# Optimization experiments

Measured on AMD Instinct MI355X. Metric: run time of the kernel, lower is better.

Reference implementation:

```python
import jax, jax.numpy as jnp
import numpy as np

C, INTER, RED4 = 256, 128, 64  # in_channels, inter_ch=max(C//2,32), C//4

def setup_inputs() -> dict:
    key = jax.random.key(0)
    ks = jax.random.split(key, 12)
    B, H, W = 8, 64, 64
    s = 0.02
    return {
        "x": jax.random.normal(ks[0], (B, C, H, W), dtype=jnp.float32),
        "theta_w": jax.random.normal(ks[1], (INTER, C), dtype=jnp.float32) * s,
        "phi_w": jax.random.normal(ks[2], (INTER, C), dtype=jnp.float32) * s,
        "g_w": jax.random.normal(ks[3], (INTER, C), dtype=jnp.float32) * s,
        "out_w": jax.random.normal(ks[4], (C, INTER), dtype=jnp.float32) * s,
        "bn_gamma": jnp.ones((C,), dtype=jnp.float32),
        "bn_beta": jnp.zeros((C,), dtype=jnp.float32),
        "fc1_w": jax.random.normal(ks[5], (RED4, C), dtype=jnp.float32) * s,
        "fc1_b": jnp.zeros((RED4,), dtype=jnp.float32),
        "fc2_w": jax.random.normal(ks[6], (C, RED4), dtype=jnp.float32) * s,
        "fc2_b": jnp.zeros((C,), dtype=jnp.float32),
    }

def reference(x, theta_w, phi_w, g_w, out_w, bn_gamma, bn_beta, fc1_w, fc1_b, fc2_w, fc2_b):
    B, Cc, H, W = x.shape
    N = H * W
    xf = x.reshape(B, Cc, N)                              # [B,C,N]
    # 1x1 convs == per-pixel matmuls
    theta = jnp.einsum('ic,bcn->bni', theta_w, xf)        # [B,N,I]
    phi = jnp.einsum('ic,bcn->bin', phi_w, xf)            # [B,I,N]
    g = jnp.einsum('ic,bcn->bni', g_w, xf)                # [B,N,I]
    scale = 1.0 / jnp.sqrt(jnp.asarray(theta.shape[-1], theta.dtype))
    attn = jax.nn.softmax(jnp.einsum('bni,bim->bnm', theta, phi) * scale, axis=-1)  # [B,N,N]
    out = jnp.einsum('bnm,bmi->bni', attn, g)             # [B,N,I]
    out = jnp.einsum('ci,bni->bcn', out_w, out).reshape(B, Cc, H, W)
    # BatchNorm2d (training mode: batch stats, biased variance, eps=1e-5)
    mean = out.mean(axis=(0, 2, 3))
    var = out.var(axis=(0, 2, 3))
    out = (out - mean[:, None, None]) * jax.lax.rsqrt(var[:, None, None] + 1e-5)
    out = out * bn_gamma[:, None, None] + bn_beta[:, None, None]
    # SE channel attention on the input x
    pooled = x.mean(axis=(2, 3))                          # [B,C]
    h = jax.nn.relu(pooled @ fc1_w.T + fc1_b)
    ch_w = jax.nn.sigmoid(h @ fc2_w.T + fc2_b)[:, :, None, None]
    return x + out * ch_w
```

## Files before the change

### kernel.cpp

```cpp
#include <hip/hip_runtime.h>

#define B_DIM 8
#define C_DIM 256
#define I_DIM 128
#define N_DIM 4096
#define R_DIM 64

typedef unsigned short u16;
typedef unsigned int u32;
typedef __attribute__((ext_vector_type(8))) __bf16 bf16x8;
typedef __attribute__((ext_vector_type(4))) float f32x4;
typedef __attribute__((ext_vector_type(16))) float f32x16;

union BF8 { u32 u[4]; bf16x8 v; };

__device__ __forceinline__ u16 f2bf(float f) {
    union { float f; u32 u; } v; v.f = f;
    u32 r = v.u + 0x7FFFu + ((v.u >> 16) & 1u);
    return (u16)(r >> 16);
}
__device__ __forceinline__ float bf2f(u16 h) {
    union { u32 u; float f; } v; v.u = (u32)h << 16; return v.f;
}
__device__ __forceinline__ u32 pk2(float a, float b) {
    return (u32)f2bf(a) | ((u32)f2bf(b) << 16);
}
__device__ __forceinline__ u32 pk2t(float a, float b) {
    union { float f; u32 u; } ua, ub; ua.f = a; ub.f = b;
    return __builtin_amdgcn_perm(ub.u, ua.u, 0x07060302u);
}
__device__ __forceinline__ void async16(const u16* g, u16* l) {
    __builtin_amdgcn_global_load_lds((const __attribute__((address_space(1))) void*)g,
                                     (__attribute__((address_space(3))) void*)l, 16, 0, 0);
}

#define TH_SCALE 0.1275204890136f

static constexpr size_t OFF_BNSUM = 0;
static constexpr size_t OFF_BNSQ  = 1024;
static constexpr size_t OFF_POOL  = 2048;
static constexpr size_t OFF_CHW   = 10240;
static constexpr size_t OFF_W3    = 18432;
static constexpr size_t OFF_OWB   = 215040;
static constexpr size_t OFF_AO0   = 280576;
static constexpr size_t OFF_AO1   = OFF_AO0 + 8388608;
static constexpr size_t OFF_THETA = OFF_AO1 + 8388608;
static constexpr size_t OFF_PHIT  = OFF_THETA + 8388608;
static constexpr size_t OFF_GT    = OFF_PHIT + 8388608;
static constexpr size_t OFF_L0    = OFF_GT + 8388608;
static constexpr size_t OFF_L1    = OFF_L0 + 131072;
static constexpr size_t OFF_OUT2  = OFF_L1 + 131072;

__global__ void prep_kernel(const float* __restrict__ tw, const float* __restrict__ pw,
                            const float* __restrict__ gw, const float* __restrict__ ow,
                            u16* __restrict__ w3, u16* __restrict__ owb,
                            float* __restrict__ bnzero, float* __restrict__ pooled) {
    int idx = blockIdx.x * 256 + threadIdx.x;
    if (idx < 512) bnzero[idx] = 0.f;
    if (idx < 2048) pooled[idx] = 0.f;
    if (idx < 3 * 32768) {
        const float* src = idx < 32768 ? tw : (idx < 65536 ? pw : gw);
        w3[idx] = f2bf(src[idx & 32767]);
    }
    if (idx < 32768) owb[idx] = f2bf(ow[idx]);
}

__global__ void se_kernel(const float* __restrict__ pooled,
                          const float* __restrict__ fc1w, const float* __restrict__ fc1b,
                          const float* __restrict__ fc2w, const float* __restrict__ fc2b,
                          float* __restrict__ chw) {
    int b = blockIdx.x, t = threadIdx.x;
    __shared__ float sp[C_DIM], sh[R_DIM];
    sp[t] = pooled[b * C_DIM + t] * (1.f / N_DIM);
    __syncthreads();
    if (t < R_DIM) {
        float a = fc1b[t];
        for (int c = 0; c < C_DIM; ++c) a += sp[c] * fc1w[t * C_DIM + c];
        sh[t] = a > 0.f ? a : 0.f;
    }
    __syncthreads();
    float a = fc2b[t];
    for (int j = 0; j < R_DIM; ++j) a += sh[j] * fc2w[t * R_DIM + j];
    chw[b * C_DIM + t] = 1.f / (1.f + __builtin_amdgcn_exp2f(-a * 1.44269504089f));
}

__global__ __launch_bounds__(256) void qkv_kernel(const float* __restrict__ x,
                                                  const u16* __restrict__ w3,
                                                  u16* __restrict__ theta,
                                                  u16* __restrict__ phiT,
                                                  u16* __restrict__ gT,
                                                  float* __restrict__ pooled) {
    const int bid = blockIdx.x;
    const int b = bid & 7, nt = bid >> 3;
    const int n0 = nt * 64;
    const int t = threadIdx.x, lane = t & 63, w = t >> 6;
    const int cl = lane & 31, h = lane >> 5;

    __shared__ u16 As[64 * 256];
    __shared__ u16 Ep[128 * 72];

    {
        const float* xb = x + ((size_t)b * C_DIM) * N_DIM + n0;
        for (int it = 0; it < 16; ++it) {
            int id = it * 256 + t;
            int c = id >> 4, l16 = id & 15;
            float4 v = *(const float4*)(xb + (size_t)c * N_DIM + l16 * 4);
            int g = c >> 3, co = c & 7;
            float vv[4] = {v.x, v.y, v.z, v.w};
            #pragma unroll
            for (int k = 0; k < 4; ++k) {
                int n = l16 * 4 + k;
                As[n * 256 + ((g ^ (n & 7)) << 3) + co] = f2bf(vv[k]);
            }
            float s = (v.x + v.y) + (v.z + v.w);
            s += __shfl_xor(s, 1); s += __shfl_xor(s, 2);
            s += __shfl_xor(s, 4); s += __shfl_xor(s, 8);
            if ((t & 15) == 0) atomicAdd(&pooled[b * C_DIM + c], s);
        }
    }
    __syncthreads();

    const int mt = w & 1;
    const int ip = w >> 1;
    bf16x8 afr[16];
    #pragma unroll
    for (int ks = 0; ks < 16; ++ks) {
        int r = mt * 32 + cl;
        int g = 2 * ks + h;
        afr[ks] = *(const bf16x8*)&As[r * 256 + ((g ^ (r & 7)) << 3)];
    }

    for (int z = 0; z < 3; ++z) {
        const u16* wz = w3 + z * (I_DIM * C_DIM);
        f32x16 acc[2] = {};
        #pragma unroll
        for (int ks = 0; ks < 16; ++ks) {
            #pragma unroll
            for (int f = 0; f < 2; ++f) {
                int irow = (2 * ip + f) * 32 + cl;
                bf16x8 bfr = *(const bf16x8*)(wz + (size_t)irow * C_DIM + ks * 16 + h * 8);
                acc[f] = __builtin_amdgcn_mfma_f32_32x32x16_bf16(afr[ks], bfr, acc[f], 0, 0, 0);
            }
        }
        if (z < 2) {
            float sc = (z == 0) ? TH_SCALE : 1.0f;
            #pragma unroll
            for (int f = 0; f < 2; ++f) {
                int i = (2 * ip + f) * 32 + cl;
                #pragma unroll
                for (int r2 = 0; r2 < 4; ++r2)
                    #pragma unroll
                    for (int e = 0; e < 4; ++e) {
                        int n = mt * 32 + 8 * r2 + 4 * h + e;
                        Ep[n * 136 + i] = f2bf(acc[f][4 * r2 + e] * sc);
                    }
            }
            __syncthreads();
            u16* dst = (z == 0) ? theta : phiT;
            #pragma unroll
            for (int it = 0; it < 4; ++it) {
                int id = it * 256 + t;
                int n = id >> 4, l16 = id & 15;
                f32x4 vv = *(const f32x4*)&Ep[n * 136 + l16 * 8];
                *(f32x4*)(dst + ((size_t)(b * N_DIM) + n0 + n) * I_DIM + l16 * 8) = vv;
            }
            __syncthreads();
        } else {
            #pragma unroll
            for (int f = 0; f < 2; ++f) {
                int i = (2 * ip + f) * 32 + cl;
                #pragma unroll
                for (int r2 = 0; r2 < 4; ++r2) {
                    u32 lo = pk2(acc[f][4 * r2 + 0], acc[f][4 * r2 + 1]);
                    u32 hi = pk2(acc[f][4 * r2 + 2], acc[f][4 * r2 + 3]);
                    int nb = mt * 32 + 8 * r2 + 4 * h;
                    *(u32*)&Ep[i * 72 + nb] = lo;
                    *(u32*)&Ep[i * 72 + nb + 2] = hi;
                }
            }
            __syncthreads();
            #pragma unroll
            for (int it = 0; it < 4; ++it) {
                int id = it * 256 + t;
                int i = id >> 3, l8 = id & 7;
                f32x4 vv = *(const f32x4*)&Ep[i * 72 + l8 * 8];
                *(f32x4*)(gT + ((size_t)(b * I_DIM) + i) * N_DIM + n0 + l8 * 8) = vv;
            }
        }
    }
}

__global__ __launch_bounds__(256) void attn_kernel(const u16* __restrict__ theta,
                                                   const u16* __restrict__ phiT,
                                                   const u16* __restrict__ gT,
                                                   u16* __restrict__ ao0, u16* __restrict__ ao1,
                                                   float* __restrict__ l0, float* __restrict__ l1) {
    const int bid = blockIdx.x;
    const int b = bid & 7, mh = (bid >> 3) & 1, qt = bid >> 4;
    const int t = threadIdx.x, lane = t & 63, w = t >> 6;
    const int cl = lane & 31, h = lane >> 5;
    const int qw = qt * 128 + w * 32;

    __shared__ u16 SM[32768];
    __shared__ float lex[4][32];

    bf16x8 qf[8];
    {
        const u16* qp = theta + ((size_t)(b * N_DIM) + qw + cl) * I_DIM + h * 8;
        #pragma unroll
        for (int ks = 0; ks < 8; ++ks) qf[ks] = *(const bf16x8*)(qp + ks * 16);
    }

    const u16* kbase = phiT + (size_t)b * N_DIM * I_DIM + (size_t)(mh * 2048) * I_DIM;
    const u16* vbase = gT + (size_t)b * I_DIM * N_DIM + mh * 2048;
    const u16* kptr[4]; const u16* vptr[4];
    #pragma unroll
    for (int it = 0; it < 4; ++it) {
        int gi = (w * 4 + it) * 64 + lane;
        int kr = gi >> 4, kg = gi & 15;
        kptr[it] = kbase + (size_t)kr * I_DIM + ((kg ^ (kr & 7)) << 3);
        int vr = gi >> 3, vg = gi & 7;
        vptr[it] = vbase + (size_t)vr * N_DIM + ((vg ^ (vr & 7)) << 3);
    }

    auto issue = [&](int p) {
        u16* Kd = SM + p * 16384;
        u16* Vd = SM + p * 16384 + 8192;
        #pragma unroll
        for (int it = 0; it < 4; ++it) { async16(kptr[it], Kd + (w * 4 + it) * 512); kptr[it] += 64 * I_DIM; }
        #pragma unroll
        for (int it = 0; it < 4; ++it) { async16(vptr[it], Vd + (w * 4 + it) * 512); vptr[it] += 64; }
    };

    float lsum = 0.f;
    f32x16 O[4] = {};

    issue(0);

    for (int mc = 0; mc < 32; ++mc) {
        const int p = mc & 1;
        __asm__ volatile("s_barrier" ::: "memory");
        if (mc < 31) {
            issue(1 - p);
            __asm__ volatile("s_waitcnt vmcnt(8)" ::: "memory");
        } else {
            __asm__ volatile("s_waitcnt vmcnt(0)" ::: "memory");
        }
        __asm__ volatile("s_barrier" ::: "memory");

        const u16* Ks = SM + p * 16384;
        const u16* Vs = SM + p * 16384 + 8192;

        u32 pk[8][2];
        #pragma unroll
        for (int mt2 = 0; mt2 < 2; ++mt2) {
            f32x16 S = {};
            #pragma unroll
            for (int ks = 0; ks < 8; ++ks) {
                int r = mt2 * 32 + cl;
                bf16x8 kf = *(const bf16x8*)&Ks[r * 128 + (((2 * ks + h) ^ (r & 7)) << 3)];
                S = __builtin_amdgcn_mfma_f32_32x32x16_bf16(kf, qf[ks], S, 0, 0, 0);
            }
            #pragma unroll
            for (int r2 = 0; r2 < 4; ++r2) {
                float p0 = __builtin_amdgcn_exp2f(S[4 * r2 + 0]);
                float p1 = __builtin_amdgcn_exp2f(S[4 * r2 + 1]);
                float p2 = __builtin_amdgcn_exp2f(S[4 * r2 + 2]);
                float p3 = __builtin_amdgcn_exp2f(S[4 * r2 + 3]);
                lsum += (p0 + p1) + (p2 + p3);
                pk[mt2 * 4 + r2][0] = pk2t(p0, p1);
                pk[mt2 * 4 + r2][1] = pk2t(p2, p3);
            }
        }

        #pragma unroll
        for (int ks = 0; ks < 4; ++ks) {
            u32 a0 = pk[2 * ks][0], a1 = pk[2 * ks][1];
            u32 b0 = pk[2 * ks + 1][0], b1 = pk[2 * ks + 1][1];
            bool hb = (h != 0);
            u32 own0 = hb ? b0 : a0, own1 = hb ? b1 : a1;
            u32 xf0 = hb ? a0 : b0, xf1 = hb ? a1 : b1;
            u32 rc0 = (u32)__shfl_xor((int)xf0, 32);
            u32 rc1 = (u32)__shfl_xor((int)xf1, 32);
            BF8 A;
            A.u[0] = hb ? rc0 : own0;
            A.u[1] = hb ? rc1 : own1;
            A.u[2] = hb ? own0 : rc0;
            A.u[3] = hb ? own1 : rc1;
            #pragma unroll
            for (int f = 0; f < 4; ++f) {
                int ir = f * 32 + cl;
                bf16x8 vf = *(const bf16x8*)&Vs[ir * 64 + (((2 * ks + h) ^ (ir & 7)) << 3)];
                O[f] = __builtin_amdgcn_mfma_f32_32x32x16_bf16(A.v, vf, O[f], 0, 0, 0);
            }
        }
    }

    lsum += __shfl_xor(lsum, 32);
    if (h == 0) lex[w][cl] = lsum;
    __asm__ volatile("s_waitcnt lgkmcnt(0)" ::: "memory");

    float linv[16];
    {
        float* lw = lex[w];
        #pragma unroll
        for (int r2 = 0; r2 < 4; ++r2) {
            f32x4 lv = *(const f32x4*)&lw[8 * r2 + 4 * h];
            #pragma unroll
            for (int e = 0; e < 4; ++e) linv[4 * r2 + e] = 1.f / lv[e];
        }
    }

    u16* aop = (mh == 0) ? ao0 : ao1;
    float* lp = (mh == 0) ? l0 : l1;
    if (h == 0) lp[(size_t)b * N_DIM + qw + cl] = lsum;

    u16* ep = SM + w * 4096;
    #pragma unroll
    for (int f = 0; f < 4; ++f)
        #pragma unroll
        for (int r2 = 0; r2 < 4; ++r2)
            #pragma unroll
            for (int e = 0; e < 4; ++e) {
                int q = 8 * r2 + 4 * h + e;
                ep[q * 128 + f * 32 + cl] = f2bf(O[f][4 * r2 + e] * linv[4 * r2 + e]);
            }
    __asm__ volatile("s_waitcnt lgkmcnt(0)" ::: "memory");
    #pragma unroll
    for (int it = 0; it < 8; ++it) {
        int id = it * 64 + lane;
        int q = id >> 4, l16 = id & 15;
        f32x4 vv = *(const f32x4*)&ep[q * 128 + l16 * 8];
        *(f32x4*)(aop + ((size_t)(b * N_DIM) + qw + q) * I_DIM + l16 * 8) = vv;
    }
}

__global__ __launch_bounds__(256) void oproj_kernel(const u16* __restrict__ ao0,
                                                    const u16* __restrict__ ao1,
                                                    const float* __restrict__ l0,
                                                    const float* __restrict__ l1,
                                                    const u16* __restrict__ owb,
                                                    u16* __restrict__ out2,
                                                    float* __restrict__ bnsum,
                                                    float* __restrict__ bnsumsq) {
    const int bid = blockIdx.x;
    const int b = bid & 7, nt = bid >> 3;
    const int n0 = nt * 64;
    const int t = threadIdx.x, lane = t & 63, w = t >> 6;
    const int cl = lane & 31, h = lane >> 5;

    __shared__ u16 Ep[256 * 72];
    __shared__ float lsum[C_DIM], lsq[C_DIM];
    lsum[t] = 0.f; lsq[t] = 0.f;
    __syncthreads();

    const int mt = w & 1;
    const int nn = n0 + mt * 32 + cl;
    float w0, w1;
    {
        float la = l0[(size_t)b * N_DIM + nn], lb = l1[(size_t)b * N_DIM + nn];
        float inv = 1.f / (la + lb);
        w0 = la * inv; w1 = lb * inv;
    }
    bf16x8 afr[8];
    {
        const u16* p0 = ao0 + ((size_t)(b * N_DIM) + nn) * I_DIM + h * 8;
        const u16* p1 = ao1 + ((size_t)(b * N_DIM) + nn) * I_DIM + h * 8;
        #pragma unroll
        for (int ks = 0; ks < 8; ++ks) {
            bf16x8 x0 = *(const bf16x8*)(p0 + ks * 16);
            bf16x8 x1 = *(const bf16x8*)(p1 + ks * 16);
            const u16* u0 = (const u16*)&x0;
            const u16* u1 = (const u16*)&x1;
            float c0 = w0 * bf2f(u0[0]) + w1 * bf2f(u1[0]);
            float c1 = w0 * bf2f(u0[1]) + w1 * bf2f(u1[1]);
            float c2 = w0 * bf2f(u0[2]) + w1 * bf2f(u1[2]);
            float c3 = w0 * bf2f(u0[3]) + w1 * bf2f(u1[3]);
            float c4 = w0 * bf2f(u0[4]) + w1 * bf2f(u1[4]);
            float c5 = w0 * bf2f(u0[5]) + w1 * bf2f(u1[5]);
            float c6 = w0 * bf2f(u0[6]) + w1 * bf2f(u1[6]);
            float c7 = w0 * bf2f(u0[7]) + w1 * bf2f(u1[7]);
            BF8 r;
            r.u[0] = pk2(c0, c1); r.u[1] = pk2(c2, c3);
            r.u[2] = pk2(c4, c5); r.u[3] = pk2(c6, c7);
            afr[ks] = r.v;
        }
    }

    f32x16 D[4] = {};
    #pragma unroll
    for (int ks = 0; ks < 8; ++ks) {
        #pragma unroll
        for (int j = 0; j < 4; ++j) {
            int cr = ((w >> 1) * 4 + j) * 32 + cl;
            bf16x8 bfr = *(const bf16x8*)(owb + (size_t)cr * I_DIM + ks * 16 + h * 8);
            D[j] = __builtin_amdgcn_mfma_f32_32x32x16_bf16(afr[ks], bfr, D[j], 0, 0, 0);
        }
    }

    #pragma unroll
    for (int j = 0; j < 4; ++j) {
        int c = ((w >> 1) * 4 + j) * 32 + cl;
        float s1 = 0.f, s2 = 0.f;
        #pragma unroll
        for (int r2 = 0; r2 < 4; ++r2) {
            float v0 = D[j][4 * r2 + 0], v1 = D[j][4 * r2 + 1];
            float v2 = D[j][4 * r2 + 2], v3 = D[j][4 * r2 + 3];
            s1 += (v0 + v1) + (v2 + v3);
            s2 += (v0 * v0 + v1 * v1) + (v2 * v2 + v3 * v3);
            int nb = mt * 32 + 8 * r2 + 4 * h;
            *(u32*)&Ep[c * 72 + nb] = pk2(v0, v1);
            *(u32*)&Ep[c * 72 + nb + 2] = pk2(v2, v3);
        }
        atomicAdd(&lsum[c], s1);
        atomicAdd(&lsq[c], s2);
    }
    __syncthreads();
    #pragma unroll
    for (int it = 0; it < 8; ++it) {
        int id = it * 256 + t;
        int c = id >> 3, l8 = id & 7;
        f32x4 vv = *(const f32x4*)&Ep[c * 72 + l8 * 8];
        *(f32x4*)(out2 + ((size_t)(b * C_DIM) + c) * N_DIM + n0 + l8 * 8) = vv;
    }
    atomicAdd(&bnsum[t], lsum[t]);
    atomicAdd(&bnsumsq[t], lsq[t]);
}

__global__ void final_kernel(const float* __restrict__ x, const u16* __restrict__ out2,
                             const float* __restrict__ bnsum, const float* __restrict__ bnsumsq,
                             const float* __restrict__ gamma, const float* __restrict__ beta,
                             const float* __restrict__ chw, float* __restrict__ out) {
    int idx = blockIdx.x * 256 + threadIdx.x;
    int e = idx * 4;
    int b = e >> 20;
    int c = (e >> 12) & 255;
    float mean = bnsum[c] * (1.f / 32768.f);
    float var = bnsumsq[c] * (1.f / 32768.f) - mean * mean;
    float sc = gamma[c] * rsqrtf(var + 1e-5f);
    float sh = beta[c] - mean * sc;
    float cw = chw[b * C_DIM + c];
    ushort4 o16 = ((const ushort4*)out2)[idx];
    float4 xv = ((const float4*)x)[idx];
    float4 res;
    res.x = xv.x + (bf2f(o16.x) * sc + sh) * cw;
    res.y = xv.y + (bf2f(o16.y) * sc + sh) * cw;
    res.z = xv.z + (bf2f(o16.z) * sc + sh) * cw;
    res.w = xv.w + (bf2f(o16.w) * sc + sh) * cw;
    ((float4*)out)[idx] = res;
}

extern "C" void kernel_launch(void* const* d_in, const int* in_sizes, int n_in,
                              void* d_out, int out_size, void* d_ws, size_t ws_size,
                              hipStream_t stream) {
    const float* x   = (const float*)d_in[0];
    const float* tw  = (const float*)d_in[1];
    const float* pw  = (const float*)d_in[2];
    const float* gw  = (const float*)d_in[3];
    const float* ow  = (const float*)d_in[4];
    const float* gam = (const float*)d_in[5];
    const float* bet = (const float*)d_in[6];
    const float* f1w = (const float*)d_in[7];
    const float* f1b = (const float*)d_in[8];
    const float* f2w = (const float*)d_in[9];
    const float* f2b = (const float*)d_in[10];
    float* out = (float*)d_out;

    char* ws = (char*)d_ws;
    float* bnsum   = (float*)(ws + OFF_BNSUM);
    float* bnsumsq = (float*)(ws + OFF_BNSQ);
    float* pooled  = (float*)(ws + OFF_POOL);
    float* chw     = (float*)(ws + OFF_CHW);
    u16*   w3      = (u16*)(ws + OFF_W3);
    u16*   owb     = (u16*)(ws + OFF_OWB);
    u16*   ao0     = (u16*)(ws + OFF_AO0);
    u16*   ao1     = (u16*)(ws + OFF_AO1);
    u16*   theta   = (u16*)(ws + OFF_THETA);
    u16*   phiT    = (u16*)(ws + OFF_PHIT);
    u16*   gT      = (u16*)(ws + OFF_GT);
    float* l0      = (float*)(ws + OFF_L0);
    float* l1      = (float*)(ws + OFF_L1);
    u16*   out2    = (u16*)(ws + OFF_OUT2);

    prep_kernel<<<384, 256, 0, stream>>>(tw, pw, gw, ow, w3, owb, bnsum, pooled);
    qkv_kernel<<<512, 256, 0, stream>>>(x, w3, theta, phiT, gT, pooled);
    se_kernel<<<B_DIM, 256, 0, stream>>>(pooled, f1w, f1b, f2w, f2b, chw);
    attn_kernel<<<512, 256, 0, stream>>>(theta, phiT, gT, ao0, ao1, l0, l1);
    oproj_kernel<<<512, 256, 0, stream>>>(ao0, ao1, l0, l1, owb, out2, bnsum, bnsumsq);
    final_kernel<<<8192, 256, 0, stream>>>(x, out2, bnsum, bnsumsq, gam, bet, chw, out);
}
```

Measured before the change: 273.8 us.

## Split attention key chunks across two wave groups and fold SE into attention

The attention kernel now runs 512 threads per block. Two groups of four waves each take half of every 64-key chunk, and their partial outputs and row sums are combined through LDS at the end. The shuffle-based P transpose is replaced with v_permlane32_swap, s_setprio is raised around the MFMA sections, and the separate SE kernel launch is folded into block 0 of the attention kernel. The aim is more waves per CU to hide latency and one fewer launch, at the cost of an extra LDS reduction, more barriers and higher LDS use.

After: 331.4 us. 1.21x slower.

```diff
diff --git a/kernel.cpp b/kernel.cpp
--- a/kernel.cpp
+++ b/kernel.cpp
@@ -32,6 +32,9 @@
 __device__ __forceinline__ void async16(const u16* g, u16* l) {
     __builtin_amdgcn_global_load_lds((const __attribute__((address_space(1))) void*)g,
                                      (__attribute__((address_space(3))) void*)l, 16, 0, 0);
+}
+__device__ __forceinline__ void plswap(u32& a, u32& b) {
+    __asm__("v_permlane32_swap_b32 %0, %1" : "+v"(a), "+v"(b));
 }
 
 #define TH_SCALE 0.1275204890136f
@@ -65,25 +68,6 @@
     if (idx < 32768) owb[idx] = f2bf(ow[idx]);
 }
 
-__global__ void se_kernel(const float* __restrict__ pooled,
-                          const float* __restrict__ fc1w, const float* __restrict__ fc1b,
-                          const float* __restrict__ fc2w, const float* __restrict__ fc2b,
-                          float* __restrict__ chw) {
-    int b = blockIdx.x, t = threadIdx.x;
-    __shared__ float sp[C_DIM], sh[R_DIM];
-    sp[t] = pooled[b * C_DIM + t] * (1.f / N_DIM);
-    __syncthreads();
-    if (t < R_DIM) {
-        float a = fc1b[t];
-        for (int c = 0; c < C_DIM; ++c) a += sp[c] * fc1w[t * C_DIM + c];
-        sh[t] = a > 0.f ? a : 0.f;
-    }
-    __syncthreads();
-    float a = fc2b[t];
-    for (int j = 0; j < R_DIM; ++j) a += sh[j] * fc2w[t * R_DIM + j];
-    chw[b * C_DIM + t] = 1.f / (1.f + __builtin_amdgcn_exp2f(-a * 1.44269504089f));
-}
-
 __global__ __launch_bounds__(256) void qkv_kernel(const float* __restrict__ x,
                                                   const u16* __restrict__ w3,
                                                   u16* __restrict__ theta,
@@ -190,19 +174,27 @@
     }
 }
 
-__global__ __launch_bounds__(256) void attn_kernel(const u16* __restrict__ theta,
-                                                   const u16* __restrict__ phiT,
-                                                   const u16* __restrict__ gT,
-                                                   u16* __restrict__ ao0, u16* __restrict__ ao1,
-                                                   float* __restrict__ l0, float* __restrict__ l1) {
+__global__ __launch_bounds__(512, 4) void attn_kernel(const u16* __restrict__ theta,
+                                                      const u16* __restrict__ phiT,
+                                                      const u16* __restrict__ gT,
+                                                      u16* __restrict__ ao0, u16* __restrict__ ao1,
+                                                      float* __restrict__ l0, float* __restrict__ l1,
+                                                      const float* __restrict__ pooled,
+                                                      const float* __restrict__ fc1w,
+                                                      const float* __restrict__ fc1b,
+                                                      const float* __restrict__ fc2w,
+                                                      const float* __restrict__ fc2b,
+                                                      float* __restrict__ chw) {
     const int bid = blockIdx.x;
     const int b = bid & 7, mh = (bid >> 3) & 1, qt = bid >> 4;
     const int t = threadIdx.x, lane = t & 63, w = t >> 6;
     const int cl = lane & 31, h = lane >> 5;
-    const int qw = qt * 128 + w * 32;
-
-    __shared__ u16 SM[32768];
-    __shared__ float lex[4][32];
+    const int wt = w & 3, kh = w >> 2;
+    const int qw = qt * 128 + wt * 32;
+
+    __shared__ __align__(16) u16 SM[34816];
+    __shared__ float lexs[8][32];
+    __shared__ float sse[512];
 
     bf16x8 qf[8];
     {
@@ -213,10 +205,10 @@
 
     const u16* kbase = phiT + (size_t)b * N_DIM * I_DIM + (size_t)(mh * 2048) * I_DIM;
     const u16* vbase = gT + (size_t)b * I_DIM * N_DIM + mh * 2048;
-    const u16* kptr[4]; const u16* vptr[4];
+    const u16* kptr[2]; const u16* vptr[2];
     #pragma unroll
-    for (int it = 0; it < 4; ++it) {
-        int gi = (w * 4 + it) * 64 + lane;
+    for (int it = 0; it < 2; ++it) {
+        int gi = (w * 2 + it) * 64 + lane;
         int kr = gi >> 4, kg = gi & 15;
         kptr[it] = kbase + (size_t)kr * I_DIM + ((kg ^ (kr & 7)) << 3);
         int vr = gi >> 3, vg = gi & 7;
@@ -225,15 +217,17 @@
 
     auto issue = [&](int p) {
         u16* Kd = SM + p * 16384;
-        u16* Vd = SM + p * 16384 + 8192;
-        #pragma unroll
-        for (int it = 0; it < 4; ++it) { async16(kptr[it], Kd + (w * 4 + it) * 512); kptr[it] += 64 * I_DIM; }
-        #pragma unroll
-        for (int it = 0; it < 4; ++it) { async16(vptr[it], Vd + (w * 4 + it) * 512); vptr[it] += 64; }
+        u16* Vd = Kd + 8192;
+        #pragma unroll
+        for (int it = 0; it < 2; ++it) { async16(kptr[it], Kd + (w * 2 + it) * 512); kptr[it] += 64 * I_DIM; }
+        #pragma unroll
+        for (int it = 0; it < 2; ++it) { async16(vptr[it], Vd + (w * 2 + it) * 512); vptr[it] += 64; }
     };
 
     float lsum = 0.f;
     f32x16 O[4] = {};
+    const int krow = kh * 32 + cl;
+    const int kswz = krow & 7;
 
     issue(0);
 
@@ -242,96 +236,147 @@
         __asm__ volatile("s_barrier" ::: "memory");
         if (mc < 31) {
             issue(1 - p);
-            __asm__ volatile("s_waitcnt vmcnt(8)" ::: "memory");
+            __asm__ volatile("s_waitcnt vmcnt(4)" ::: "memory");
         } else {
             __asm__ volatile("s_waitcnt vmcnt(0)" ::: "memory");
         }
         __asm__ volatile("s_barrier" ::: "memory");
 
         const u16* Ks = SM + p * 16384;
-        const u16* Vs = SM + p * 16384 + 8192;
-
-        u32 pk[8][2];
-        #pragma unroll
-        for (int mt2 = 0; mt2 < 2; ++mt2) {
-            f32x16 S = {};
-            #pragma unroll
-            for (int ks = 0; ks < 8; ++ks) {
-                int r = mt2 * 32 + cl;
-                bf16x8 kf = *(const bf16x8*)&Ks[r * 128 + (((2 * ks + h) ^ (r & 7)) << 3)];
-                S = __builtin_amdgcn_mfma_f32_32x32x16_bf16(kf, qf[ks], S, 0, 0, 0);
-            }
-            #pragma unroll
-            for (int r2 = 0; r2 < 4; ++r2) {
-                float p0 = __builtin_amdgcn_exp2f(S[4 * r2 + 0]);
-                float p1 = __builtin_amdgcn_exp2f(S[4 * r2 + 1]);
-                float p2 = __builtin_amdgcn_exp2f(S[4 * r2 + 2]);
-                float p3 = __builtin_amdgcn_exp2f(S[4 * r2 + 3]);
-                lsum += (p0 + p1) + (p2 + p3);
-                pk[mt2 * 4 + r2][0] = pk2t(p0, p1);
-                pk[mt2 * 4 + r2][1] = pk2t(p2, p3);
-            }
-        }
-
-        #pragma unroll
-        for (int ks = 0; ks < 4; ++ks) {
-            u32 a0 = pk[2 * ks][0], a1 = pk[2 * ks][1];
-            u32 b0 = pk[2 * ks + 1][0], b1 = pk[2 * ks + 1][1];
-            bool hb = (h != 0);
-            u32 own0 = hb ? b0 : a0, own1 = hb ? b1 : a1;
-            u32 xf0 = hb ? a0 : b0, xf1 = hb ? a1 : b1;
-            u32 rc0 = (u32)__shfl_xor((int)xf0, 32);
-            u32 rc1 = (u32)__shfl_xor((int)xf1, 32);
+        const u16* Vs = Ks + 8192;
+
+        f32x16 S = {};
+        __builtin_amdgcn_s_setprio(1);
+        #pragma unroll
+        for (int ks = 0; ks < 8; ++ks) {
+            bf16x8 kf = *(const bf16x8*)&Ks[krow * 128 + (((2 * ks + h) ^ kswz) << 3)];
+            S = __builtin_amdgcn_mfma_f32_32x32x16_bf16(kf, qf[ks], S, 0, 0, 0);
+        }
+        __builtin_amdgcn_s_setprio(0);
+
+        u32 pk[4][2];
+        #pragma unroll
+        for (int r2 = 0; r2 < 4; ++r2) {
+            float p0 = __builtin_amdgcn_exp2f(S[4 * r2 + 0]);
+            float p1 = __builtin_amdgcn_exp2f(S[4 * r2 + 1]);
+            float p2 = __builtin_amdgcn_exp2f(S[4 * r2 + 2]);
+            float p3 = __builtin_amdgcn_exp2f(S[4 * r2 + 3]);
+            lsum += (p0 + p1) + (p2 + p3);
+            pk[r2][0] = pk2t(p0, p1);
+            pk[r2][1] = pk2t(p2, p3);
+        }
+
+        __builtin_amdgcn_s_setprio(1);
+        #pragma unroll
+        for (int s = 0; s < 2; ++s) {
+            u32 x0 = pk[2 * s][0], y0 = pk[2 * s + 1][0];
+            u32 x1 = pk[2 * s][1], y1 = pk[2 * s + 1][1];
+            plswap(x0, y0);
+            plswap(x1, y1);
             BF8 A;
-            A.u[0] = hb ? rc0 : own0;
-            A.u[1] = hb ? rc1 : own1;
-            A.u[2] = hb ? own0 : rc0;
-            A.u[3] = hb ? own1 : rc1;
+            A.u[0] = x0; A.u[1] = x1; A.u[2] = y0; A.u[3] = y1;
+            const int g = 4 * kh + 2 * s + h;
             #pragma unroll
             for (int f = 0; f < 4; ++f) {
                 int ir = f * 32 + cl;
-                bf16x8 vf = *(const bf16x8*)&Vs[ir * 64 + (((2 * ks + h) ^ (ir & 7)) << 3)];
+                bf16x8 vf = *(const bf16x8*)&Vs[ir * 64 + ((g ^ (ir & 7)) << 3)];
                 O[f] = __builtin_amdgcn_mfma_f32_32x32x16_bf16(A.v, vf, O[f], 0, 0, 0);
             }
         }
-    }
-
-    lsum += __shfl_xor(lsum, 32);
-    if (h == 0) lex[w][cl] = lsum;
-    __asm__ volatile("s_waitcnt lgkmcnt(0)" ::: "memory");
-
-    float linv[16];
+        __builtin_amdgcn_s_setprio(0);
+    }
+
     {
-        float* lw = lex[w];
-        #pragma unroll
-        for (int r2 = 0; r2 < 4; ++r2) {
-            f32x4 lv = *(const f32x4*)&lw[8 * r2 + 4 * h];
-            #pragma unroll
-            for (int e = 0; e < 4; ++e) linv[4 * r2 + e] = 1.f / lv[e];
-        }
-    }
+        union { float f; u32 u; } a, b2;
+        a.f = lsum; b2.f = lsum;
+        plswap(a.u, b2.u);
+        lsum = a.f + b2.f;
+    }
+    if (h == 0) lexs[w][cl] = lsum;
+    __syncthreads();
+
+    float* ep32 = (float*)SM;
+    float* slot = ep32 + ((wt << 6) + lane) * 68;
+    if (kh == 0) {
+        #pragma unroll
+        for (int f = 0; f < 4; ++f)
+            #pragma unroll
+            for (int r2 = 0; r2 < 4; ++r2) {
+                f32x4 vv = {O[f][4 * r2 + 0], O[f][4 * r2 + 1], O[f][4 * r2 + 2], O[f][4 * r2 + 3]};
+                *(f32x4*)(slot + f * 16 + r2 * 4) = vv;
+            }
+    }
+    __syncthreads();
 
     u16* aop = (mh == 0) ? ao0 : ao1;
     float* lp = (mh == 0) ? l0 : l1;
-    if (h == 0) lp[(size_t)b * N_DIM + qw + cl] = lsum;
-
-    u16* ep = SM + w * 4096;
-    #pragma unroll
-    for (int f = 0; f < 4; ++f)
-        #pragma unroll
-        for (int r2 = 0; r2 < 4; ++r2)
-            #pragma unroll
-            for (int e = 0; e < 4; ++e) {
-                int q = 8 * r2 + 4 * h + e;
-                ep[q * 128 + f * 32 + cl] = f2bf(O[f][4 * r2 + e] * linv[4 * r2 + e]);
-            }
-    __asm__ volatile("s_waitcnt lgkmcnt(0)" ::: "memory");
-    #pragma unroll
-    for (int it = 0; it < 8; ++it) {
-        int id = it * 64 + lane;
-        int q = id >> 4, l16 = id & 15;
-        f32x4 vv = *(const f32x4*)&ep[q * 128 + l16 * 8];
-        *(f32x4*)(aop + ((size_t)(b * N_DIM) + qw + q) * I_DIM + l16 * 8) = vv;
+
+    if (kh == 1) {
+        if (h == 0) lp[(size_t)b * N_DIM + qw + cl] = lexs[wt][cl] + lexs[wt + 4][cl];
+        float linv[16];
+        #pragma unroll
+        for (int r2 = 0; r2 < 4; ++r2) {
+            f32x4 la = *(const f32x4*)&lexs[wt][8 * r2 + 4 * h];
+            f32x4 lb = *(const f32x4*)&lexs[wt + 4][8 * r2 + 4 * h];
+            #pragma unroll
+            for (int e = 0; e < 4; ++e) linv[4 * r2 + e] = 1.f / (la[e] + lb[e]);
+        }
+        #pragma unroll
+        for (int f = 0; f < 4; ++f)
+            #pragma unroll
+            for (int r2 = 0; r2 < 4; ++r2) {
+                f32x4 pv = *(const f32x4*)(slot + f * 16 + r2 * 4);
+                #pragma unroll
+                for (int e = 0; e < 4; ++e)
+                    O[f][4 * r2 + e] = (O[f][4 * r2 + e] + pv[e]) * linv[4 * r2 + e];
+            }
+    }
+    __syncthreads();
+
+    if (kh == 1) {
+        u16* ep = SM + wt * 4096;
+        #pragma unroll
+        for (int f = 0; f < 4; ++f)
+            #pragma unroll
+            for (int r2 = 0; r2 < 4; ++r2)
+                #pragma unroll
+                for (int e = 0; e < 4; ++e) {
+                    int q = 8 * r2 + 4 * h + e;
+                    ep[q * 128 + f * 32 + cl] = f2bf(O[f][4 * r2 + e]);
+                }
+        __asm__ volatile("s_waitcnt lgkmcnt(0)" ::: "memory");
+        #pragma unroll
+        for (int it = 0; it < 8; ++it) {
+            int id = it * 64 + lane;
+            int q = id >> 4, l16 = id & 15;
+            f32x4 vv = *(const f32x4*)&ep[q * 128 + l16 * 8];
+            *(f32x4*)(aop + ((size_t)(b * N_DIM) + qw + q) * I_DIM + l16 * 8) = vv;
+        }
+    }
+
+    if (bid == 0) {
+        const int sb = t >> 6;
+        const int j = t & 63;
+        float d = 0.f;
+        for (int c = 0; c < C_DIM; c += 4) {
+            float4 pv = *(const float4*)(pooled + sb * C_DIM + c);
+            float4 wv = *(const float4*)(fc1w + j * C_DIM + c);
+            d += (pv.x * wv.x + pv.y * wv.y) + (pv.z * wv.z + pv.w * wv.w);
+        }
+        float a = fc1b[j] + d * (1.f / N_DIM);
+        sse[sb * 64 + j] = a > 0.f ? a : 0.f;
+        __syncthreads();
+        #pragma unroll
+        for (int r = 0; r < 4; ++r) {
+            int c = j * 4 + r;
+            float acc = fc2b[c];
+            for (int k = 0; k < R_DIM; k += 4) {
+                float4 wv = *(const float4*)(fc2w + c * 64 + k);
+                acc += (sse[sb * 64 + k] * wv.x + sse[sb * 64 + k + 1] * wv.y)
+                     + (sse[sb * 64 + k + 2] * wv.z + sse[sb * 64 + k + 3] * wv.w);
+            }
+            chw[sb * C_DIM + c] = 1.f / (1.f + __builtin_amdgcn_exp2f(-acc * 1.44269504089f));
+        }
     }
 }
 
@@ -484,8 +529,8 @@
 
     prep_kernel<<<384, 256, 0, stream>>>(tw, pw, gw, ow, w3, owb, bnsum, pooled);
     qkv_kernel<<<512, 256, 0, stream>>>(x, w3, theta, phiT, gT, pooled);
-    se_kernel<<<B_DIM, 256, 0, stream>>>(pooled, f1w, f1b, f2w, f2b, chw);
-    attn_kernel<<<512, 256, 0, stream>>>(theta, phiT, gT, ao0, ao1, l0, l1);
+    attn_kernel<<<512, 512, 0, stream>>>(theta, phiT, gT, ao0, ao1, l0, l1,
+                                         pooled, f1w, f1b, f2w, f2b, chw);
     oproj_kernel<<<512, 256, 0, stream>>>(ao0, ao1, l0, l1, owb, out2, bnsum, bnsumsq);
     final_kernel<<<8192, 256, 0, stream>>>(x, out2, bnsum, bnsumsq, gam, bet, chw, out);
 }
```
